# Optimization experiments

Measured on AMD Instinct MI355X. Metric: run time of the kernel, lower is better.

## Reference

```python
import jax, jax.numpy as jnp
import numpy as np

N_USERS = 27094
M_SPOTS = 42852
D = 128
E_US = 600000
E_SP = 500000
L = 3  # num_layers


def setup_inputs() -> dict:
    key = jax.random.key(0)
    ks = jax.random.split(key, 16)
    spot_emb = jax.random.normal(ks[0], (M_SPOTS, D), jnp.float32) * 0.1
    user_emb = jax.random.normal(ks[1], (N_USERS, D), jnp.float32) * 0.1
    W_spot = jax.random.normal(ks[2], (D, D), jnp.float32) / np.sqrt(D)
    W_spot10 = jax.random.normal(ks[3], (D, D), jnp.float32) / np.sqrt(D)
    W_spot20 = jax.random.normal(ks[4], (D, D), jnp.float32) / np.sqrt(D)
    user_spot = jnp.stack([
        jax.random.randint(ks[5], (E_US,), 0, N_USERS, jnp.int32),
        jax.random.randint(ks[6], (E_US,), 0, M_SPOTS, jnp.int32),
    ])
    def mk_graph(k1, k2, k3):
        ei = jnp.stack([
            jax.random.randint(k1, (E_SP,), 0, M_SPOTS, jnp.int32),
            jax.random.randint(k2, (E_SP,), 0, M_SPOTS, jnp.int32),
        ])
        ew = jax.random.uniform(k3, (E_SP,), jnp.float32)
        return ei, ew
    spot_edge_index, spot_edge_weight = mk_graph(ks[7], ks[8], ks[9])
    spot10_edge_index, spot10_edge_weight = mk_graph(ks[10], ks[11], ks[12])
    spot20_edge_index, spot20_edge_weight = mk_graph(ks[13], ks[14], ks[15])
    return {
        'spot_emb': spot_emb, 'user_emb': user_emb,
        'W_spot': W_spot, 'W_spot10': W_spot10, 'W_spot20': W_spot20,
        'spot_edge_weight': spot_edge_weight, 'spot10_edge_weight': spot10_edge_weight,
        'spot20_edge_weight': spot20_edge_weight,
        'user_spot': user_spot, 'spot_edge_index': spot_edge_index,
        'spot10_edge_index': spot10_edge_index, 'spot20_edge_index': spot20_edge_index,
    }


def _gcn_light(x, W, ei, ew, n):
    # GCNConv semantics with given edge weights, no self loops, no bias:
    # x' = xW; deg = scatter(ew, dst); out = sum_e dinv[src]*ew*dinv[dst] * x'[src]
    xw = x @ W
    deg = jax.ops.segment_sum(ew, ei[1], num_segments=n)
    dinv = jnp.where(deg > 0, jax.lax.rsqrt(jnp.maximum(deg, 1e-12)), 0.0)
    norm = dinv[ei[0]] * ew * dinv[ei[1]]
    return jax.ops.segment_sum(norm[:, None] * xw[ei[0]], ei[1], num_segments=n)


def _propagate(spot_x, user_x, u, s, inv_div):
    # LightGCN bipartite propagation with symmetric sqrt(deg_u*deg_s) norm,
    # accumulating the mean over layer outputs (incl. layer 0).
    spot_acc, user_acc = spot_x, user_x
    for _ in range(L):
        user_new = jax.ops.segment_sum(spot_x[s] * inv_div, u, num_segments=N_USERS)
        spot_new = jax.ops.segment_sum(user_x[u] * inv_div, s, num_segments=M_SPOTS)
        spot_x, user_x = spot_new, user_new
        spot_acc = spot_acc + spot_x
        user_acc = user_acc + user_x
    inv = 1.0 / (L + 1)
    return spot_acc * inv, user_acc * inv, spot_x, user_x


def reference(spot_emb, user_emb, W_spot, W_spot10, W_spot20,
              spot_edge_weight, spot10_edge_weight, spot20_edge_weight,
              user_spot, spot_edge_index, spot10_edge_index, spot20_edge_index):
    u, s = user_spot[0], user_spot[1]
    ones = jnp.ones((u.shape[0],), jnp.float32)
    udeg = jax.ops.segment_sum(ones, u, num_segments=N_USERS)
    sdeg = jax.ops.segment_sum(ones, s, num_segments=M_SPOTS)
    inv_div = (1.0 / jnp.sqrt(udeg[u] * sdeg[s]))[:, None]  # [E_US,1]

    # branch 1: spot_x1 includes the category conv before propagation
    cat1 = _gcn_light(spot_emb, W_spot, spot_edge_index, spot_edge_weight, M_SPOTS)
    so1, uo1, _, _ = _propagate(spot_emb + cat1, user_emb, u, s, inv_div)

    # branches 2 and 3 propagate raw embeddings (conv output only added to the
    # accumulator's layer-0 term in the original code), so share one propagation
    p_s, p_u, fin_s, _ = _propagate(spot_emb, user_emb, u, s, inv_div)
    cat2 = _gcn_light(spot_emb, W_spot10, spot10_edge_index, spot10_edge_weight, M_SPOTS)
    so2 = p_s + cat2 / (L + 1)
    uo2 = p_u
    # original code (faithfully) feeds the post-loop spot_x2 into spot_conv20
    cat3 = _gcn_light(fin_s, W_spot20, spot20_edge_index, spot20_edge_weight, M_SPOTS)
    so3 = p_s + cat3 / (L + 1)
    uo3 = p_u
    return (so1, uo1, so2, uo2, so3, uo3)
```

## Files before the change

### kernel.cpp

```cpp
#include <hip/hip_runtime.h>
#include <hip/hip_fp16.h>

#define D 128
#define SU 56
#define SS 40
#define SG 36
typedef unsigned int uint;
typedef unsigned short ushort;
typedef unsigned long long ull;

__device__ __forceinline__ float blo(uint u) { return __uint_as_float(u << 16); }
__device__ __forceinline__ float bhi(uint u) { return __uint_as_float(u & 0xffff0000u); }
__device__ __forceinline__ uint bpack(float a, float b) {
  uint ua = __float_as_uint(a), ub = __float_as_uint(b);
  ua = (ua + 0x7fffu + ((ua >> 16) & 1u)) >> 16;
  ub = (ub + 0x7fffu + ((ub >> 16) & 1u)) & 0xffff0000u;
  return ua | ub;
}
__device__ __forceinline__ float h2f(ushort h) { return __half2float(__ushort_as_half(h)); }
__device__ __forceinline__ ushort f2h(float f) { return __half_as_ushort(__float2half(f)); }

#define PKSCALE 16777216.0f
#define PKMASK ((1ULL << 40) - 1)

__device__ __forceinline__ float gdinv_of(ull pk) {
  float d = (float)(pk & PKMASK) * (1.0f / PKSCALE);
  return d > 0.f ? rsqrtf(fmaxf(d, 1e-12f)) : 0.f;
}
__device__ __forceinline__ float cdinv(int c) {
  return c > 0 ? rsqrtf((float)c) : 0.f;
}

struct DualHi { const uint4* p; };
__device__ __forceinline__ float4 ldx(const float* X, size_t i) {
  return ((const float4*)X)[i];
}
__device__ __forceinline__ float4 ldx(DualHi X, size_t i) {
  uint4 v = X.p[i];
  return make_float4(blo(v.z), bhi(v.z), blo(v.w), bhi(v.w));
}

template <typename XT>
__device__ __forceinline__ void gemm_body(int blk, XT X, const float* __restrict__ W,
                                          ushort* __restrict__ Y, int rows) {
  int tid = threadIdx.x;
  int c = tid & 31, rg = tid >> 5;
  int r0 = blk * 32 + rg * 4;
  float4 acc[4];
#pragma unroll
  for (int j = 0; j < 4; ++j) acc[j] = make_float4(0.f, 0.f, 0.f, 0.f);
  for (int k4 = 0; k4 < 32; ++k4) {
    float4 xv[4];
#pragma unroll
    for (int j = 0; j < 4; ++j) {
      int r = r0 + j;
      if (r >= rows) r = rows - 1;
      xv[j] = ldx(X, (size_t)r * 32 + k4);
    }
#pragma unroll
    for (int kk = 0; kk < 4; ++kk) {
      float4 wv = ((const float4*)W)[(k4 * 4 + kk) * 32 + c];
#pragma unroll
      for (int j = 0; j < 4; ++j) {
        float xs = kk == 0 ? xv[j].x : kk == 1 ? xv[j].y : kk == 2 ? xv[j].z : xv[j].w;
        acc[j].x = fmaf(xs, wv.x, acc[j].x);
        acc[j].y = fmaf(xs, wv.y, acc[j].y);
        acc[j].z = fmaf(xs, wv.z, acc[j].z);
        acc[j].w = fmaf(xs, wv.w, acc[j].w);
      }
    }
  }
#pragma unroll
  for (int j = 0; j < 4; ++j) {
    int r = r0 + j;
    if (r < rows)
      ((uint2*)(Y + (size_t)r * D))[c] =
          make_uint2(bpack(acc[j].x, acc[j].y), bpack(acc[j].z, acc[j].w));
  }
}

__global__ __launch_bounds__(256) void k_build(
    const int* __restrict__ uu, const int* __restrict__ ss, int EUS,
    const int* __restrict__ ei1, const int* __restrict__ ei2, const int* __restrict__ ei3,
    const float* __restrict__ ew1, const float* __restrict__ ew2,
    const float* __restrict__ ew3, int ES1, int ES2, int ES3,
    int* cnt_u, int* cnt_s, ushort* __restrict__ ue_s, ushort* __restrict__ se_u,
    ull* gpk, uint* __restrict__ grec, int AM, int M, int nbBip, int nbG,
    const float* __restrict__ se, const float* __restrict__ W1, ushort* __restrict__ xw) {
  int b = blockIdx.x;
  if (b < nbBip) {
    int e = b * 256 + threadIdx.x;
    if (e >= EUS) return;
    int ui = uu[e], si = ss[e];
    int p = atomicAdd(&cnt_u[ui], 1);
    if (p < SU) ue_s[(size_t)ui * SU + p] = (ushort)si;
    int q = atomicAdd(&cnt_s[si], 1);
    if (q < SS) se_u[(size_t)si * SS + q] = (ushort)ui;
  } else if (b < nbBip + nbG) {
    int t = (b - nbBip) * 256 + threadIdx.x;
    const int* ei; const float* ew; int g, le, ESg;
    if (t < ES1) { g = 0; le = t; ei = ei1; ew = ew1; ESg = ES1; }
    else if (t < ES1 + ES2) { g = 1; le = t - ES1; ei = ei2; ew = ew2; ESg = ES2; }
    else if (t < ES1 + ES2 + ES3) { g = 2; le = t - ES1 - ES2; ei = ei3; ew = ew3; ESg = ES3; }
    else return;
    int src = ei[le], dst = ei[ESg + le];
    float w = ew[le];
    ull pk = (1ULL << 40) | (ull)(uint)(w * PKSCALE);
    ull old = atomicAdd(&gpk[(size_t)g * AM + dst], pk);
    int p = (int)(old >> 40);
    if (p < SG) grec[((size_t)g * M + dst) * SG + p] = (uint)src | ((uint)f2h(w) << 16);
  } else {
    gemm_body(b - nbBip - nbG, se, W1, xw, M);
  }
}

__device__ __forceinline__ void gcn_body(int gblk, const ull* __restrict__ gpkg,
                                         const uint* __restrict__ grecg,
                                         const ushort* __restrict__ xw,
                                         const float* __restrict__ base,
                                         float* __restrict__ out, uint* outSC,
                                         const int* __restrict__ cnt_sd,
                                         float scale, int M) {
  int g = gblk * 256 + threadIdx.x;
  int row = g >> 6, l = g & 63;
  if (row >= M) return;
  ull mypk = gpkg[row];
  int cv = (int)(mypk >> 40);
  if (cv > SG) cv = SG;
  float dr = gdinv_of(mypk);
  const uint* rec = grecg + (size_t)row * SG;
  const uint* sv = (const uint*)xw;
  float2 sum = make_float2(0.f, 0.f);
#pragma unroll 4
  for (int i = 0; i < cv; ++i) {
    uint r = rec[i];
    int sr = (int)(r & 0xffffu);
    float w = h2f((ushort)(r >> 16)) * gdinv_of(gpkg[sr]);
    uint v = sv[(size_t)sr * 64 + l];
    sum.x = fmaf(w, blo(v), sum.x);
    sum.y = fmaf(w, bhi(v), sum.y);
  }
  float sc = dr * scale;
  size_t lf = (size_t)row * 64 + l;
  float2 b = ((const float2*)base)[lf];
  float2 o = make_float2(fmaf(sc, sum.x, b.x), fmaf(sc, sum.y, b.y));
  ((float2*)out)[lf] = o;
  if (outSC) {
    float sd = cdinv(cnt_sd[row]);
    outSC[(size_t)row * 128 + 4 * (l >> 1) + (l & 1)] = bpack(sd * o.x, sd * o.y);
  }
}

__global__ __launch_bounds__(256) void k_mid(
    const ull* __restrict__ gpk, const uint* __restrict__ grec,
    const ushort* __restrict__ xw, const float* __restrict__ spot_emb,
    float* __restrict__ o_so1, uint* __restrict__ SC, const int* __restrict__ cnt_s,
    int M, int nbGg1,
    const float* __restrict__ ue, const int* __restrict__ cnt_u,
    uint4* __restrict__ UC, int N) {
  int b = blockIdx.x;
  if (b < nbGg1) {
    gcn_body(b, gpk, grec, xw, spot_emb, o_so1, SC, cnt_s, 1.0f, M);
    return;
  }
  int g = (b - nbGg1) * 256 + threadIdx.x;
  int row = g >> 5, lane = g & 31;
  if (row < N) {
    float d = cdinv(cnt_u[row]);
    float4 v = ((const float4*)ue)[(size_t)row * 32 + lane];
    uint a = bpack(d * v.x, d * v.y), bq = bpack(d * v.z, d * v.w);
    UC[(size_t)row * 32 + lane] = make_uint4(a, bq, a, bq);
  } else if (row < N + M) {
    int r = row - N;
    float d = cdinv(cnt_s[r]);
    float4 v = ((const float4*)spot_emb)[(size_t)r * 32 + lane];
    ((uint2*)SC)[(size_t)r * 64 + 2 * lane + 1] =
        make_uint2(bpack(d * v.x, d * v.y), bpack(d * v.z, d * v.w));
  }
}

__global__ __launch_bounds__(256) void k_prop(
    const int* __restrict__ cnt_u, const ushort* __restrict__ ue_s,
    const int* __restrict__ cnt_s, const ushort* __restrict__ se_u,
    const uint2* __restrict__ SCin, const uint2* __restrict__ UCin,
    uint2* __restrict__ SCout, uint2* __restrict__ UCout,
    const float* __restrict__ base_u1, const float* __restrict__ base_u2,
    const float* __restrict__ base_s1, const float* __restrict__ base_s2,
    float* __restrict__ acc_u1, float* __restrict__ acc_u2,
    float* __restrict__ acc_s1, float* __restrict__ acc_s2,
    float* dup_u2, float* dup_s2, float fs, int finalLayer, int N, int M,
    int nbProp, const float* __restrict__ Xg, const float* __restrict__ Wg,
    ushort* __restrict__ xwg) {
  int b = blockIdx.x;
  if (b >= nbProp) {
    if (Wg) gemm_body(b - nbProp, Xg, Wg, xwg, M);
    return;
  }
  int g = b * 256 + threadIdx.x;
  int row = g >> 6, l = g & 63;
  const ushort* ei; const uint2* tbl;
  uint2* otbl; const float *b1, *b2; float *a1, *a2, *d2; float wrow; int r, cv;
  if (row < N) {
    r = row; cv = cnt_u[r]; if (cv > SU) cv = SU;
    ei = ue_s + (size_t)r * SU; tbl = SCin; otbl = UCout;
    b1 = base_u1; b2 = base_u2; a1 = acc_u1; a2 = acc_u2; d2 = dup_u2;
  } else if (row < N + M) {
    r = row - N; cv = cnt_s[r]; if (cv > SS) cv = SS;
    ei = se_u + (size_t)r * SS; tbl = UCin; otbl = SCout;
    b1 = base_s1; b2 = base_s2; a1 = acc_s1; a2 = acc_s2; d2 = dup_s2;
  } else return;
  wrow = cdinv(cv);
  float4 sum = make_float4(0.f, 0.f, 0.f, 0.f);
#pragma unroll 4
  for (int i = 0; i < cv; ++i) {
    int idx = ei[i];
    uint2 v = tbl[(size_t)idx * 64 + l];
    sum.x += blo(v.x); sum.y += bhi(v.x);
    sum.z += blo(v.y); sum.w += bhi(v.y);
  }
  if (otbl) {
    float f = finalLayer ? wrow : wrow * wrow;
    otbl[(size_t)r * 64 + l] =
        make_uint2(bpack(f * sum.x, f * sum.y), bpack(f * sum.z, f * sum.w));
  }
  int j = l >> 1, sig = l & 1;
  size_t lf = (size_t)r * 32 + j;
  const float* bb = sig ? b2 : b1;
  float* a = sig ? a2 : a1;
  float4 vb = ((const float4*)bb)[lf];
  float4 o = make_float4((vb.x + wrow * sum.x) * fs, (vb.y + wrow * sum.y) * fs,
                         (vb.z + wrow * sum.z) * fs, (vb.w + wrow * sum.w) * fs);
  ((float4*)a)[lf] = o;
  if (sig && d2) ((float4*)d2)[lf] = o;
}

__global__ __launch_bounds__(256) void k_tail(
    int gG, DualHi X3, const float* __restrict__ W3, ushort* __restrict__ xw3, int rows,
    const ull* __restrict__ gpk2, const uint* __restrict__ grec2,
    const ushort* __restrict__ xw2, float* __restrict__ o_so2, float scale, int M) {
  int b = blockIdx.x;
  if (b < gG) gemm_body(b, X3, W3, xw3, rows);
  else gcn_body(b - gG, gpk2, grec2, xw2, o_so2, o_so2, (uint*)nullptr,
                (const int*)nullptr, scale, M);
}

__global__ __launch_bounds__(256) void k_gg(
    const ull* __restrict__ gpkg, const uint* __restrict__ grecg,
    const ushort* __restrict__ xw, const float* __restrict__ base,
    float* __restrict__ out, float scale, int M) {
  gcn_body(blockIdx.x, gpkg, grecg, xw, base, out, (uint*)nullptr,
           (const int*)nullptr, scale, M);
}

extern "C" void kernel_launch(void* const* d_in, const int* in_sizes, int n_in,
                              void* d_out, int out_size, void* d_ws, size_t ws_size,
                              hipStream_t stream) {
  const float* spot_emb = (const float*)d_in[0];
  const float* user_emb = (const float*)d_in[1];
  const float* W1 = (const float*)d_in[2];
  const float* W2 = (const float*)d_in[3];
  const float* W3 = (const float*)d_in[4];
  const float* ew1 = (const float*)d_in[5];
  const float* ew2 = (const float*)d_in[6];
  const float* ew3 = (const float*)d_in[7];
  const int* us = (const int*)d_in[8];
  const int* ei1 = (const int*)d_in[9];
  const int* ei2 = (const int*)d_in[10];
  const int* ei3 = (const int*)d_in[11];

  const int M = in_sizes[0] / D;
  const int N = in_sizes[1] / D;
  const int EUS = in_sizes[8] / 2;
  const int ES1 = in_sizes[9] / 2;
  const int ES2 = in_sizes[10] / 2;
  const int ES3 = in_sizes[11] / 2;
  const int EStot = ES1 + ES2 + ES3;

  const int* uu = us;
  const int* ss = us + EUS;

  const size_t MD = (size_t)M * D, ND = (size_t)N * D;
  const int AM = (int)((M + 63) & ~63);

  float* cur = (float*)d_ws;
  auto take = [&](size_t nfloats) {
    float* p = cur; cur += (nfloats + 63) & ~(size_t)63; return p;
  };

  int* cnt_u = (int*)take(N);
  int* cnt_s = (int*)take(M);
  ull* gpk = (ull*)take((size_t)6 * AM);
  float* zero_end = cur;
  ushort* ue_s = (ushort*)take(((size_t)N * SU + 1) / 2);
  ushort* se_u = (ushort*)take(((size_t)M * SS + 1) / 2);
  uint* grec = (uint*)take((size_t)3 * M * SG);
  ushort* xw = (ushort*)take(MD / 2);
  uint2* UC_A = (uint2*)take(ND);
  uint2* UC_B = (uint2*)take(ND);
  uint2* SC_A = (uint2*)take(MD);
  uint2* SC_B = (uint2*)take(MD);

  ushort* xw3 = (ushort*)UC_A;

  float* out = (float*)d_out;
  float* o_so1 = out;
  float* o_uo1 = o_so1 + MD;
  float* o_so2 = o_uo1 + ND;
  float* o_uo2 = o_so2 + MD;
  float* o_so3 = o_uo2 + ND;
  float* o_uo3 = o_so3 + MD;

  const int B = 256;
  auto gr = [&](size_t work) { return (int)((work + B - 1) / B); };
  const int nbBip = gr(EUS);
  const int nbG = gr(EStot);
  const int nbPack = gr((size_t)(N + M) * 32);
  const int gProp = gr((size_t)(N + M) * 64);
  const int gM64 = gr((size_t)M * 64);
  const int gG = (M + 31) / 32;
  float* nulf = (float*)nullptr;

  hipMemsetAsync(cnt_u, 0, (char*)zero_end - (char*)cnt_u, stream);

  k_build<<<nbBip + nbG + gG, B, 0, stream>>>(
      uu, ss, EUS, ei1, ei2, ei3, ew1, ew2, ew3, ES1, ES2, ES3,
      cnt_u, cnt_s, ue_s, se_u, gpk, grec, AM, M, nbBip, nbG, spot_emb, W1, xw);

  k_mid<<<gM64 + nbPack, B, 0, stream>>>(gpk, grec, xw, spot_emb, o_so1, (uint*)SC_A,
                                         cnt_s, M, gM64, user_emb, cnt_u,
                                         (uint4*)UC_A, N);

  k_prop<<<gProp + gG, B, 0, stream>>>(
      cnt_u, ue_s, cnt_s, se_u, SC_A, UC_A, SC_B, UC_B,
      user_emb, user_emb, o_so1, spot_emb, o_uo1, o_uo2, o_so1, o_so2,
      nulf, nulf, 1.0f, 0, N, M, gProp, spot_emb, W2, xw);
  k_prop<<<gProp, B, 0, stream>>>(
      cnt_u, ue_s, cnt_s, se_u, SC_B, UC_B, SC_A, UC_A,
      o_uo1, o_uo2, o_so1, o_so2, o_uo1, o_uo2, o_so1, o_so2,
      nulf, nulf, 1.0f, 0, N, M, gProp, nulf, nulf, (ushort*)nullptr);
  k_prop<<<gProp, B, 0, stream>>>(
      cnt_u, ue_s, cnt_s, se_u, SC_A, UC_A, SC_B, (uint2*)nullptr,
      o_uo1, o_uo2, o_so1, o_so2, o_uo1, o_uo2, o_so1, o_so2,
      o_uo3, o_so3, 0.25f, 1, N, M, gProp, nulf, nulf, (ushort*)nullptr);

  k_tail<<<gG + gM64, B, 0, stream>>>(gG, DualHi{(const uint4*)SC_B}, W3, xw3, M,
                                      gpk + AM, grec + (size_t)M * SG, xw,
                                      o_so2, 0.25f, M);
  k_gg<<<gM64, B, 0, stream>>>(gpk + (size_t)2 * AM, grec + (size_t)2 * M * SG,
                               xw3, o_so3, o_so3, 0.25f, M);
}
```

Measured before the change: 763.9 us.

## Defer fp32 accumulator updates to final layer and shrink shared-branch tables

The propagation kernel no longer reads and writes the fp32 mean accumulators in every layer. Instead, the final layer rebuilds the accumulated sum from the stored bf16 per-layer tables, rescaled by sqrt(degree). Tables that hold identical data for both branches (the user table and the branch-2 spot table) are now stored at single width rather than duplicated, which halves their gather traffic. The cost is more index bookkeeping in the kernel, plus extra bf16 rounding on intermediate layer terms, and the final layer does extra reads to compensate.

```diff
diff --git a/kernel.cpp b/kernel.cpp
--- a/kernel.cpp
+++ b/kernel.cpp
@@ -31,13 +31,13 @@
   return c > 0 ? rsqrtf((float)c) : 0.f;
 }
 
-struct DualHi { const uint4* p; };
+struct SingleTbl { const uint2* p; };
 __device__ __forceinline__ float4 ldx(const float* X, size_t i) {
   return ((const float4*)X)[i];
 }
-__device__ __forceinline__ float4 ldx(DualHi X, size_t i) {
-  uint4 v = X.p[i];
-  return make_float4(blo(v.z), bhi(v.z), blo(v.w), bhi(v.w));
+__device__ __forceinline__ float4 ldx(SingleTbl X, size_t i) {
+  uint2 v = X.p[i];
+  return make_float4(blo(v.x), bhi(v.x), blo(v.y), bhi(v.y));
 }
 
 template <typename XT>
@@ -157,7 +157,7 @@
     float* __restrict__ o_so1, uint* __restrict__ SC, const int* __restrict__ cnt_s,
     int M, int nbGg1,
     const float* __restrict__ ue, const int* __restrict__ cnt_u,
-    uint4* __restrict__ UC, int N) {
+    uint2* __restrict__ UCs, int N) {
   int b = blockIdx.x;
   if (b < nbGg1) {
     gcn_body(b, gpk, grec, xw, spot_emb, o_so1, SC, cnt_s, 1.0f, M);
@@ -168,8 +168,8 @@
   if (row < N) {
     float d = cdinv(cnt_u[row]);
     float4 v = ((const float4*)ue)[(size_t)row * 32 + lane];
-    uint a = bpack(d * v.x, d * v.y), bq = bpack(d * v.z, d * v.w);
-    UC[(size_t)row * 32 + lane] = make_uint4(a, bq, a, bq);
+    UCs[(size_t)row * 32 + lane] =
+        make_uint2(bpack(d * v.x, d * v.y), bpack(d * v.z, d * v.w));
   } else if (row < N + M) {
     int r = row - N;
     float d = cdinv(cnt_s[r]);
@@ -182,14 +182,17 @@
 __global__ __launch_bounds__(256) void k_prop(
     const int* __restrict__ cnt_u, const ushort* __restrict__ ue_s,
     const int* __restrict__ cnt_s, const ushort* __restrict__ se_u,
-    const uint2* __restrict__ SCin, const uint2* __restrict__ UCin,
-    uint2* __restrict__ SCout, uint2* __restrict__ UCout,
-    const float* __restrict__ base_u1, const float* __restrict__ base_u2,
-    const float* __restrict__ base_s1, const float* __restrict__ base_s2,
-    float* __restrict__ acc_u1, float* __restrict__ acc_u2,
-    float* __restrict__ acc_s1, float* __restrict__ acc_s2,
-    float* dup_u2, float* dup_s2, float fs, int finalLayer, int N, int M,
-    int nbProp, const float* __restrict__ Xg, const float* __restrict__ Wg,
+    const uint2* __restrict__ uG, int uGs,
+    const uint2* __restrict__ sG, int sGs,
+    uint2* uO, int uOs, uint2* sO, int sOs,
+    int finalLayer,
+    const uint2* __restrict__ uT1, int uT1s, const uint2* __restrict__ uT2, int uT2s,
+    const uint2* __restrict__ sT1, int sT1s, const uint2* __restrict__ sT2, int sT2s,
+    const float* __restrict__ bu1, const float* __restrict__ bu2,
+    const float* __restrict__ bs1, const float* __restrict__ bs2,
+    float* au1, float* au2, float* as1, float* as2, float* du2, float* ds2,
+    int N, int M, int nbProp,
+    const float* __restrict__ Xg, const float* __restrict__ Wg,
     ushort* __restrict__ xwg) {
   int b = blockIdx.x;
   if (b >= nbProp) {
@@ -198,44 +201,68 @@
   }
   int g = b * 256 + threadIdx.x;
   int row = g >> 6, l = g & 63;
-  const ushort* ei; const uint2* tbl;
-  uint2* otbl; const float *b1, *b2; float *a1, *a2, *d2; float wrow; int r, cv;
-  if (row < N) {
-    r = row; cv = cnt_u[r]; if (cv > SU) cv = SU;
-    ei = ue_s + (size_t)r * SU; tbl = SCin; otbl = UCout;
-    b1 = base_u1; b2 = base_u2; a1 = acc_u1; a2 = acc_u2; d2 = dup_u2;
-  } else if (row < N + M) {
-    r = row - N; cv = cnt_s[r]; if (cv > SS) cv = SS;
-    ei = se_u + (size_t)r * SS; tbl = UCin; otbl = SCout;
-    b1 = base_s1; b2 = base_s2; a1 = acc_s1; a2 = acc_s2; d2 = dup_s2;
-  } else return;
-  wrow = cdinv(cv);
-  float4 sum = make_float4(0.f, 0.f, 0.f, 0.f);
+  if (row >= N + M) return;
+  bool isU = row < N;
+  int r = isU ? row : row - N;
+  int cv = isU ? cnt_u[r] : cnt_s[r];
+  int S = isU ? SU : SS;
+  if (cv > S) cv = S;
+  const ushort* ei = isU ? (ue_s + (size_t)r * SU) : (se_u + (size_t)r * SS);
+  const uint2* G = isU ? uG : sG;
+  int Gs = isU ? uGs : sGs;
+  int j = l >> 1, sig = l & 1;
+  float w = cdinv(cv);
+  float4 s = make_float4(0.f, 0.f, 0.f, 0.f);
+  if (Gs) {
 #pragma unroll 4
-  for (int i = 0; i < cv; ++i) {
-    int idx = ei[i];
-    uint2 v = tbl[(size_t)idx * 64 + l];
-    sum.x += blo(v.x); sum.y += bhi(v.x);
-    sum.z += blo(v.y); sum.w += bhi(v.y);
-  }
-  if (otbl) {
-    float f = finalLayer ? wrow : wrow * wrow;
-    otbl[(size_t)r * 64 + l] =
-        make_uint2(bpack(f * sum.x, f * sum.y), bpack(f * sum.z, f * sum.w));
-  }
-  int j = l >> 1, sig = l & 1;
-  size_t lf = (size_t)r * 32 + j;
-  const float* bb = sig ? b2 : b1;
-  float* a = sig ? a2 : a1;
-  float4 vb = ((const float4*)bb)[lf];
-  float4 o = make_float4((vb.x + wrow * sum.x) * fs, (vb.y + wrow * sum.y) * fs,
-                         (vb.z + wrow * sum.z) * fs, (vb.w + wrow * sum.w) * fs);
-  ((float4*)a)[lf] = o;
-  if (sig && d2) ((float4*)d2)[lf] = o;
+    for (int i = 0; i < cv; ++i) {
+      uint2 v = G[(size_t)ei[i] * 32 + j];
+      s.x += blo(v.x); s.y += bhi(v.x); s.z += blo(v.y); s.w += bhi(v.y);
+    }
+  } else {
+#pragma unroll 4
+    for (int i = 0; i < cv; ++i) {
+      uint2 v = G[(size_t)ei[i] * 64 + l];
+      s.x += blo(v.x); s.y += bhi(v.x); s.z += blo(v.y); s.w += bhi(v.y);
+    }
+  }
+  uint2 v1 = make_uint2(0, 0), v2 = make_uint2(0, 0);
+  if (finalLayer) {
+    const uint2* T1 = isU ? uT1 : sT1;
+    int t1s = isU ? uT1s : sT1s;
+    const uint2* T2 = isU ? uT2 : sT2;
+    int t2s = isU ? uT2s : sT2s;
+    v1 = T1[t1s ? ((size_t)r * 32 + j) : ((size_t)r * 64 + l)];
+    v2 = T2[t2s ? ((size_t)r * 32 + j) : ((size_t)r * 64 + l)];
+  }
+  uint2* O = isU ? uO : sO;
+  int Os = isU ? uOs : sOs;
+  float f = finalLayer ? w : w * w;
+  if (O) {
+    uint2 e = make_uint2(bpack(f * s.x, f * s.y), bpack(f * s.z, f * s.w));
+    if (Os) {
+      if (!sig) O[(size_t)r * 32 + j] = e;
+    } else {
+      O[(size_t)r * 64 + l] = e;
+    }
+  }
+  if (!finalLayer) return;
+  float winv = sqrtf((float)cv);
+  const float* bp = isU ? (sig ? bu2 : bu1) : (sig ? bs2 : bs1);
+  float4 base = ((const float4*)bp)[(size_t)r * 32 + j];
+  float4 acc;
+  acc.x = (base.x + winv * (blo(v1.x) + blo(v2.x)) + w * s.x) * 0.25f;
+  acc.y = (base.y + winv * (bhi(v1.x) + bhi(v2.x)) + w * s.y) * 0.25f;
+  acc.z = (base.z + winv * (blo(v1.y) + blo(v2.y)) + w * s.z) * 0.25f;
+  acc.w = (base.w + winv * (bhi(v1.y) + bhi(v2.y)) + w * s.w) * 0.25f;
+  float* ap = isU ? (sig ? au2 : au1) : (sig ? as2 : as1);
+  ((float4*)ap)[(size_t)r * 32 + j] = acc;
+  float* dp = isU ? du2 : ds2;
+  if (sig && dp) ((float4*)dp)[(size_t)r * 32 + j] = acc;
 }
 
 __global__ __launch_bounds__(256) void k_tail(
-    int gG, DualHi X3, const float* __restrict__ W3, ushort* __restrict__ xw3, int rows,
+    int gG, SingleTbl X3, const float* __restrict__ W3, ushort* __restrict__ xw3, int rows,
     const ull* __restrict__ gpk2, const uint* __restrict__ grec2,
     const ushort* __restrict__ xw2, float* __restrict__ o_so2, float scale, int M) {
   int b = blockIdx.x;
@@ -301,6 +328,7 @@
   uint2* SC_B = (uint2*)take(MD);
 
   ushort* xw3 = (ushort*)UC_A;
+  uint2* FIN = SC_B + (size_t)M * 32;
 
   float* out = (float*)d_out;
   float* o_so1 = out;
@@ -319,6 +347,7 @@
   const int gM64 = gr((size_t)M * 64);
   const int gG = (M + 31) / 32;
   float* nulf = (float*)nullptr;
+  const uint2* nult = (const uint2*)nullptr;
 
   hipMemsetAsync(cnt_u, 0, (char*)zero_end - (char*)cnt_u, stream);
 
@@ -327,23 +356,26 @@
       cnt_u, cnt_s, ue_s, se_u, gpk, grec, AM, M, nbBip, nbG, spot_emb, W1, xw);
 
   k_mid<<<gM64 + nbPack, B, 0, stream>>>(gpk, grec, xw, spot_emb, o_so1, (uint*)SC_A,
-                                         cnt_s, M, gM64, user_emb, cnt_u,
-                                         (uint4*)UC_A, N);
+                                         cnt_s, M, gM64, user_emb, cnt_u, UC_A, N);
 
   k_prop<<<gProp + gG, B, 0, stream>>>(
-      cnt_u, ue_s, cnt_s, se_u, SC_A, UC_A, SC_B, UC_B,
-      user_emb, user_emb, o_so1, spot_emb, o_uo1, o_uo2, o_so1, o_so2,
-      nulf, nulf, 1.0f, 0, N, M, gProp, spot_emb, W2, xw);
+      cnt_u, ue_s, cnt_s, se_u, SC_A, 0, UC_A, 1, UC_B, 0, SC_B, 1, 0,
+      nult, 0, nult, 0, nult, 0, nult, 0,
+      nulf, nulf, nulf, nulf, nulf, nulf, nulf, nulf, nulf, nulf,
+      N, M, gProp, spot_emb, W2, xw);
   k_prop<<<gProp, B, 0, stream>>>(
-      cnt_u, ue_s, cnt_s, se_u, SC_B, UC_B, SC_A, UC_A,
-      o_uo1, o_uo2, o_so1, o_so2, o_uo1, o_uo2, o_so1, o_so2,
-      nulf, nulf, 1.0f, 0, N, M, gProp, nulf, nulf, (ushort*)nullptr);
+      cnt_u, ue_s, cnt_s, se_u, SC_B, 1, UC_B, 0, UC_A, 1, SC_A, 0, 0,
+      nult, 0, nult, 0, nult, 0, nult, 0,
+      nulf, nulf, nulf, nulf, nulf, nulf, nulf, nulf, nulf, nulf,
+      N, M, gProp, nulf, nulf, (ushort*)nullptr);
   k_prop<<<gProp, B, 0, stream>>>(
-      cnt_u, ue_s, cnt_s, se_u, SC_A, UC_A, SC_B, (uint2*)nullptr,
-      o_uo1, o_uo2, o_so1, o_so2, o_uo1, o_uo2, o_so1, o_so2,
-      o_uo3, o_so3, 0.25f, 1, N, M, gProp, nulf, nulf, (ushort*)nullptr);
-
-  k_tail<<<gG + gM64, B, 0, stream>>>(gG, DualHi{(const uint4*)SC_B}, W3, xw3, M,
+      cnt_u, ue_s, cnt_s, se_u, SC_A, 0, UC_A, 1, (uint2*)nullptr, 0, FIN, 1, 1,
+      UC_B, 0, UC_A, 1, SC_B, 1, SC_A, 0,
+      user_emb, user_emb, o_so1, spot_emb,
+      o_uo1, o_uo2, o_so1, o_so2, o_uo3, o_so3,
+      N, M, gProp, nulf, nulf, (ushort*)nullptr);
+
+  k_tail<<<gG + gM64, B, 0, stream>>>(gG, SingleTbl{FIN}, W3, xw3, M,
                                       gpk + AM, grec + (size_t)M * SG, xw,
                                       o_so2, 0.25f, M);
   k_gg<<<gM64, B, 0, stream>>>(gpk + (size_t)2 * AM, grec + (size_t)2 * M * SG,
```

After: 713.8 us. -6.6%, faster.
